# Kernel optimization log

Measured on AMD Instinct MI355X. Metric: run time of the kernel, lower is better.

## Reference

```python
import jax, jax.numpy as jnp
import numpy as np

BETA = 0.25


def setup_inputs() -> dict:
    key = jax.random.key(0)
    k1, k2, k3, k4 = jax.random.split(key, 4)
    B, D, T, H, W = 2, 256, 8, 32, 32
    K = 8192
    z = jax.random.normal(k1, (B, D, T, H, W), dtype=jnp.float32)
    # nn.init.normal_(embedding.weight, mean=0, std=emb_dim ** -0.5)
    emb_w = jax.random.normal(k2, (K, D), dtype=jnp.float32) * (D ** -0.5)
    # torch Linear default init ~ U(-1/sqrt(in), 1/sqrt(in)); scaled normal is fine for a reference
    w1 = jax.random.normal(k3, (D, D), dtype=jnp.float32) * (D ** -0.5)
    w2 = jax.random.normal(k4, (D, D), dtype=jnp.float32) * (D ** -0.5)
    return {"z": z, "emb_w": emb_w, "w1": w1, "w2": w2}


def reference(z, emb_w, w1, w2):
    B, D, T, H, W = z.shape
    K = emb_w.shape[0]
    # permute to channels-last and flatten: [B,T,H,W,D] -> [N,D]
    z_cl = jnp.transpose(z, (0, 2, 3, 4, 1))
    z_flat = z_cl.reshape(-1, D)
    N = z_flat.shape[0]
    # simvq: Linear -> GELU (exact) -> Linear, both bias-free
    quant_codebook = jax.nn.gelu(emb_w @ w1.T, approximate=False) @ w2.T  # [K, D]
    # pairwise squared L2 distances [N, K]
    d = (
        jnp.sum(z_flat ** 2, axis=1, keepdims=True)
        + jnp.sum(quant_codebook ** 2, axis=1)
        - 2.0 * (z_flat @ quant_codebook.T)
    )
    mean_distance = jnp.mean(d)
    idx = jnp.argmin(d, axis=1)  # [N]
    # gather == one-hot @ codebook
    z_q_flat = quant_codebook[idx]  # [N, D]
    z_q = z_q_flat.reshape(z_cl.shape)
    # VQ loss with stop-gradients
    loss = jnp.mean((jax.lax.stop_gradient(z_q) - z_cl) ** 2) + BETA * jnp.mean(
        (z_q - jax.lax.stop_gradient(z_cl)) ** 2
    )
    # straight-through estimator
    z_q = z_cl + jax.lax.stop_gradient(z_q - z_cl)
    # perplexity from code usage histogram (== mean of one-hot encodings)
    counts = jnp.zeros((K,), dtype=jnp.float32).at[idx].add(1.0)
    e_mean = counts / N
    perplexity = jnp.exp(-jnp.sum(e_mean * jnp.log(e_mean + 1e-10)))
    # back to channels-first [B, D, T, H, W]
    z_q = jnp.transpose(z_q, (0, 4, 1, 2, 3))
    return z_q, loss, perplexity, mean_distance
```

## Files before the change

### kernel.cpp

```cpp
#include <hip/hip_runtime.h>
#include <math.h>

#define BATCH 2
#define DIM   256
#define THW   8192
#define NTOK  16384
#define KCB   8192
#define OUTQ  4194304
#define CAP   2000000
#define SCAP  5600

typedef short short8 __attribute__((ext_vector_type(8)));
typedef float f32x4 __attribute__((ext_vector_type(4)));

__device__ __forceinline__ unsigned short f2bf_rn(float v) {
    unsigned u = __float_as_uint(v);
    unsigned r = u + 0x7FFFu + ((u >> 16) & 1u);
    return (unsigned short)(r >> 16);
}
__device__ __forceinline__ float bf2f(unsigned short b) {
    return __uint_as_float((unsigned)b << 16);
}
__device__ __forceinline__ void gl2lds16(const unsigned short* g, unsigned short* l) {
    __builtin_amdgcn_global_load_lds(
        (const __attribute__((address_space(1))) void*)g,
        (__attribute__((address_space(3))) void*)l, 16, 0, 0);
}

__global__ void k_buildA(const float* __restrict__ z,
                         unsigned short* __restrict__ Ahi,
                         unsigned short* __restrict__ Alo,
                         float* __restrict__ zsq,
                         float* __restrict__ sA, float* __restrict__ sB,
                         float* __restrict__ partialZ) {
    __shared__ ushort2 tile[64][65];
    __shared__ float zacc[64];
    __shared__ float lacc[64];
    __shared__ float pz[256];
    int t = threadIdx.x;
    int n0 = blockIdx.x * 64;
    int b = n0 >> 13;
    int thw0 = n0 & 8191;
    if (t < 64) { zacc[t] = 0.f; lacc[t] = 0.f; }
    pz[t] = 0.f;
    __syncthreads();
    int nn_r = t & 63, dg = t >> 6;
    float a1 = 0.f, a2 = 0.f;
    for (int dc = 0; dc < 256; dc += 64) {
        for (int r = 0; r < 16; ++r) {
            int dd = r * 4 + dg;
            float v = z[((size_t)(b * 256 + dc + dd)) * 8192 + thw0 + nn_r];
            unsigned short hb = f2bf_rn(v);
            float hf = bf2f(hb);
            unsigned short lb = f2bf_rn(v - hf);
            float lf = bf2f(lb);
            tile[dd][nn_r] = make_ushort2(hb, lb);
            a1 += v * v;
            a2 += lf * lf;
        }
        __syncthreads();
        int kk = t & 63, ng = t >> 6;
        float dimsum = 0.f;
        for (int i2 = 0; i2 < 16; ++i2) {
            int nn = ng + i2 * 4;
            ushort2 hl = tile[kk][nn];
            size_t base = (size_t)(n0 + nn) * 256;
            Ahi[base + dc + kk] = hl.x;
            Alo[base + dc + kk] = hl.y;
            dimsum += bf2f(hl.x) + bf2f(hl.y);
        }
        atomicAdd(&pz[dc + kk], dimsum);
        __syncthreads();
    }
    atomicAdd(&zacc[nn_r], a1);
    atomicAdd(&lacc[nn_r], a2);
    __syncthreads();
    if (t < 64) {
        zsq[n0 + t] = zacc[t];
        sA[n0 + t] = 2.1f * sqrtf(lacc[t]);
        sB[n0 + t] = 2.1f * sqrtf(zacc[t]);
    }
    partialZ[blockIdx.x * 256 + t] = pz[t];
}

__global__ void k_splitW(const float* __restrict__ w1, const float* __restrict__ w2,
                         unsigned short* __restrict__ W1s, unsigned short* __restrict__ W2s) {
    int bid = blockIdx.x;
    int row = bid & 255;
    const float* src = (bid >> 8) ? w2 : w1;
    unsigned short* dst = ((bid >> 8) ? W2s : W1s) + (size_t)row * 768;
    int t = threadIdx.x;
    float v = src[row * 256 + t];
    unsigned short hb = f2bf_rn(v);
    unsigned short lb = f2bf_rn(v - bf2f(hb));
    dst[t] = hb;
    dst[256 + t] = hb;
    dst[512 + t] = lb;
}

__global__ void k_buildE(const float* __restrict__ emb, unsigned short* __restrict__ E) {
    int t = threadIdx.x;
    int row = blockIdx.x * 4 + (t >> 6);
    int e4 = (t & 63) * 4;
    float4 v = *(const float4*)&emb[(size_t)row * 256 + e4];
    ushort4 hi, lo;
    hi.x = f2bf_rn(v.x); lo.x = f2bf_rn(v.x - bf2f(hi.x));
    hi.y = f2bf_rn(v.y); lo.y = f2bf_rn(v.y - bf2f(hi.y));
    hi.z = f2bf_rn(v.z); lo.z = f2bf_rn(v.z - bf2f(hi.z));
    hi.w = f2bf_rn(v.w); lo.w = f2bf_rn(v.w - bf2f(hi.w));
    size_t base = (size_t)row * 768;
    *(ushort4*)&E[base + e4] = hi;
    *(ushort4*)&E[base + 256 + e4] = lo;
    *(ushort4*)&E[base + 512 + e4] = hi;
}

template <int GELU>
__global__ __launch_bounds__(256) void k_mlp(const unsigned short* __restrict__ A,
                                             const unsigned short* __restrict__ B,
                                             unsigned short* __restrict__ Hs,
                                             float* __restrict__ C_t) {
    __shared__ __align__(16) char smem[32768];
    unsigned short* Asm = (unsigned short*)smem;
    unsigned short* Bsm = (unsigned short*)(smem + 16384);

    int t = threadIdx.x;
    int lane = t & 63;
    int w = t >> 6;
    int wm = w >> 1, wn = w & 1;
    int m0 = blockIdx.y * 128;
    int n0 = blockIdx.x * 128;

    int rA = w * 8 + (lane >> 3);
    int ch_l = lane & 7;
    int ch_g = ch_l ^ (lane >> 3);
    const unsigned short* gA = A + (size_t)(m0 + rA) * 768 + ch_g * 8;
    const unsigned short* gB = B + (size_t)(n0 + rA) * 768 + ch_g * 8;
    unsigned short* lA = &Asm[rA * 64 + ch_l * 8];
    unsigned short* lB = &Bsm[rA * 64 + ch_l * 8];

    f32x4 acc[4][4];
#pragma unroll
    for (int i = 0; i < 4; ++i)
#pragma unroll
        for (int j = 0; j < 4; ++j)
            acc[i][j] = f32x4{0.f, 0.f, 0.f, 0.f};

#pragma unroll
    for (int i = 0; i < 4; ++i) {
        gl2lds16(gA + (size_t)(32 * i) * 768, lA + 32 * i * 64);
        gl2lds16(gB + (size_t)(32 * i) * 768, lB + 32 * i * 64);
    }
    __syncthreads();

    int l15 = lane & 15;
    int quad = lane >> 4;
    int sw = l15 & 7;
    for (int kc = 0; kc < 12; ++kc) {
#pragma unroll
        for (int kk = 0; kk < 2; ++kk) {
            short8 a[4], b[4];
#pragma unroll
            for (int i = 0; i < 4; ++i)
                a[i] = *(const short8*)&Asm[(wm * 64 + i * 16 + l15) * 64 +
                                            (((kk * 4 + quad) ^ sw) * 8)];
#pragma unroll
            for (int j = 0; j < 4; ++j)
                b[j] = *(const short8*)&Bsm[(wn * 64 + j * 16 + l15) * 64 +
                                            (((kk * 4 + quad) ^ sw) * 8)];
#pragma unroll
            for (int i = 0; i < 4; ++i)
#pragma unroll
                for (int j = 0; j < 4; ++j)
                    acc[i][j] = __builtin_amdgcn_mfma_f32_16x16x32_bf16(a[i], b[j], acc[i][j], 0, 0, 0);
        }
        __syncthreads();
        if (kc < 11) {
            int ko = (kc + 1) * 64;
#pragma unroll
            for (int i = 0; i < 4; ++i) {
                gl2lds16(gA + (size_t)(32 * i) * 768 + ko, lA + 32 * i * 64);
                gl2lds16(gB + (size_t)(32 * i) * 768 + ko, lB + 32 * i * 64);
            }
            __syncthreads();
        }
    }

#pragma unroll
    for (int i = 0; i < 4; ++i) {
#pragma unroll
        for (int reg = 0; reg < 4; ++reg) {
            int mrow = m0 + wm * 64 + i * 16 + quad * 4 + reg;
#pragma unroll
            for (int j = 0; j < 4; ++j) {
                int ncol = n0 + wn * 64 + j * 16 + l15;
                float h = acc[i][j][reg];
                if (GELU) {
                    float g = 0.5f * h * (1.f + erff(h * 0.70710678118654752f));
                    unsigned short hb = f2bf_rn(g);
                    unsigned short lb = f2bf_rn(g - bf2f(hb));
                    size_t base = (size_t)mrow * 768;
                    Hs[base + ncol] = hb;
                    Hs[base + 256 + ncol] = lb;
                    Hs[base + 512 + ncol] = hb;
                } else {
                    C_t[(size_t)mrow * 8192 + ncol] = h;
                }
            }
        }
    }
}

__global__ void k_buildB(const float* __restrict__ C_t,
                         unsigned short* __restrict__ Bhi,
                         unsigned short* __restrict__ Blo,
                         float* __restrict__ csq,
                         float* __restrict__ sC, float* __restrict__ sCl,
                         unsigned* __restrict__ tileMaxC, unsigned* __restrict__ tileMaxCl,
                         float* __restrict__ accums, float* __restrict__ partialC) {
    __shared__ ushort2 tile[64][65];
    __shared__ float kacc[64];
    __shared__ float lacc[64];
    __shared__ float pc[256];
    int t = threadIdx.x;
    int k0 = blockIdx.x * 64;
    if (t < 64) { kacc[t] = 0.f; lacc[t] = 0.f; }
    pc[t] = 0.f;
    __syncthreads();
    int nn_r = t & 63, dg = t >> 6;
    float a1 = 0.f, a2 = 0.f;
    for (int dc = 0; dc < 256; dc += 64) {
        for (int r = 0; r < 16; ++r) {
            int dd = r * 4 + dg;
            float v = C_t[(size_t)(dc + dd) * KCB + k0 + nn_r];
            unsigned short hb = f2bf_rn(v);
            float hf = bf2f(hb);
            unsigned short lb = f2bf_rn(v - hf);
            float lf = bf2f(lb);
            tile[dd][nn_r] = make_ushort2(hb, lb);
            a1 += v * v;
            a2 += lf * lf;
        }
        __syncthreads();
        int kk = t & 63, ng = t >> 6;
        float dimsum = 0.f;
        for (int i2 = 0; i2 < 16; ++i2) {
            int nn = ng + i2 * 4;
            ushort2 hl = tile[kk][nn];
            size_t base = (size_t)(k0 + nn) * 256;
            Bhi[base + dc + kk] = hl.x;
            Blo[base + dc + kk] = hl.y;
            dimsum += bf2f(hl.x) + bf2f(hl.y);
        }
        atomicAdd(&pc[dc + kk], dimsum);
        __syncthreads();
    }
    atomicAdd(&kacc[nn_r], a1);
    atomicAdd(&lacc[nn_r], a2);
    __syncthreads();
    if (t < 64) {
        float c2 = kacc[t], l2 = lacc[t];
        float sc = sqrtf(c2), sl = sqrtf(l2);
        csq[k0 + t] = c2;
        sC[k0 + t] = sc;
        sCl[k0 + t] = sl;
        int tl = blockIdx.x >> 1;
        atomicMax(&tileMaxC[tl], __float_as_uint(sc));
        atomicMax(&tileMaxCl[tl], __float_as_uint(sl));
        atomicMax((unsigned*)&accums[3], __float_as_uint(c2));
        atomicMax((unsigned*)&accums[4], __float_as_uint(l2));
    }
    partialC[blockIdx.x * 256 + t] = pc[t];
}

__global__ __launch_bounds__(512, 2) void k_dist_hi(const unsigned short* __restrict__ A,
                                                    const unsigned short* __restrict__ B,
                                                    const float* __restrict__ zsq,
                                                    const float* __restrict__ csq,
                                                    const float* __restrict__ sA,
                                                    const float* __restrict__ sB,
                                                    const unsigned* __restrict__ tileMaxC,
                                                    const unsigned* __restrict__ tileMaxCl,
                                                    unsigned long long* __restrict__ packed,
                                                    float* __restrict__ accums,
                                                    unsigned long long* __restrict__ cand) {
    __shared__ __align__(16) char smem[98304];
    float* sbd     = (float*)smem;
    float* gprev_s = (float*)(smem + 2048);
    float* thr     = (float*)(smem + 3072);
    unsigned* scnt  = (unsigned*)(smem + 4096);
    unsigned* sbase = (unsigned*)(smem + 4100);
    unsigned long long* scand = (unsigned long long*)(smem + 4112);

    int t = threadIdx.x;
    int lane = t & 63;
    int w = t >> 6;
    int wm = w >> 1, wn = w & 1;

    unsigned f = blockIdx.x + (blockIdx.y << 6);
    unsigned xcd = f & 7, i5 = f >> 3;
    unsigned mb = (xcd & 3) * 16 + (i5 & 15);
    unsigned nb = (xcd >> 2) * 16 + (i5 >> 4);
    int m0 = (int)mb * 256;
    int n0 = (int)nb * 256;

    int rsrow = t >> 2;
    int rch = (t & 3) ^ (rsrow & 3);
    const unsigned short* gA0 = A + (size_t)(m0 + rsrow) * 256 + rch * 8;
    const unsigned short* gB0 = B + (size_t)(n0 + rsrow) * 256 + rch * 8;
    unsigned short* smemU = (unsigned short*)smem;

    int l15 = lane & 15;
    int quad = lane >> 4;
    int sw2 = l15 & 3;

    float M1 = sqrtf(accums[3]);
    float M2 = sqrtf(accums[4]);
    float msC  = fmaxf(__uint_as_float(tileMaxC[2 * nb]),
                       __uint_as_float(tileMaxC[2 * nb + 1]));
    float msCl = fmaxf(__uint_as_float(tileMaxCl[2 * nb]),
                       __uint_as_float(tileMaxCl[2 * nb + 1]));

    f32x4 acc[4][8];
#pragma unroll
    for (int i = 0; i < 4; ++i)
#pragma unroll
        for (int j = 0; j < 8; ++j)
            acc[i][j] = f32x4{0.f, 0.f, 0.f, 0.f};

#define STAGE(b, koff)                                                      \
    {                                                                       \
        unsigned short* base_ = smemU + (b) * 16384;                        \
        gl2lds16(gA0 + (koff), base_ + t * 8);                              \
        gl2lds16(gA0 + 128 * 256 + (koff), base_ + 4096 + t * 8);           \
        gl2lds16(gB0 + (koff), base_ + 8192 + t * 8);                       \
        gl2lds16(gB0 + 128 * 256 + (koff), base_ + 12288 + t * 8);          \
    }

#define KSTEP(KC, BUF, WN, DOSTAGE)                                         \
    {                                                                       \
        __builtin_amdgcn_sched_barrier(0);                                  \
        __builtin_amdgcn_s_barrier();   \
        __builtin_amdgcn_sched_barrier(0);                                  \
        if (DOSTAGE) STAGE(((KC) + 2) % 3, ((KC) + 2) * 32);                \
        asm volatile("s_waitcnt vmcnt(" #WN ")" ::: "memory");              \
        __builtin_amdgcn_sched_barrier(0);                                  \
        __builtin_amdgcn_s_barrier();           \
        __builtin_amdgcn_sched_barrier(0);                                  \
        const unsigned short* Ar = smemU + (BUF) * 16384;                   \
        const unsigned short* Br = Ar + 8192;                               \
        short8 a[4], b[8];                                                  \
        _Pragma("unroll")                                                   \
        for (int i = 0; i < 4; ++i)                                         \
            a[i] = *(const short8*)&Ar[(wm * 64 + i * 16 + l15) * 32 +      \
                                       ((quad ^ sw2) * 8)];                 \
        _Pragma("unroll")                                                   \
        for (int j = 0; j < 8; ++j)                                         \
            b[j] = *(const short8*)&Br[(wn * 128 + j * 16 + l15) * 32 +     \
                                       ((quad ^ sw2) * 8)];                 \
        __builtin_amdgcn_s_setprio(1);                                      \
        _Pragma("unroll")                                                   \
        for (int i = 0; i < 4; ++i)                                         \
            _Pragma("unroll")                                               \
            for (int j = 0; j < 8; ++j)                                     \
                acc[i][j] = __builtin_amdgcn_mfma_f32_16x16x32_bf16(        \
                    a[i], b[j], acc[i][j], 0, 0, 0);                        \
        __builtin_amdgcn_s_setprio(0);                                      \
    }

    STAGE(0, 0)
    STAGE(1, 32)
    KSTEP(0, 0, 8, 1)
    KSTEP(1, 1, 8, 1)
    KSTEP(2, 2, 8, 1)
    KSTEP(3, 0, 8, 1)
    KSTEP(4, 1, 8, 1)
    KSTEP(5, 2, 8, 1)
    KSTEP(6, 0, 4, 0)
    KSTEP(7, 1, 0, 0)
#undef KSTEP
#undef STAGE
    __syncthreads();

    float cv[8];
    int cols[8];
#pragma unroll
    for (int j = 0; j < 8; ++j) {
        int cloc = wn * 128 + j * 16 + l15;
        cols[j] = n0 + cloc;
        cv[j] = csq[cols[j]];
    }

    if (t == 0) *scnt = 0;
    if (t < 256) {
        const unsigned* hp = (const unsigned*)&packed[m0 + t];
        gprev_s[t] = __uint_as_float(__atomic_load_n(hp + 1, __ATOMIC_RELAXED));
    }
#pragma unroll
    for (int i = 0; i < 4; ++i) {
#pragma unroll
        for (int reg = 0; reg < 4; ++reg) {
            int rloc = wm * 64 + i * 16 + quad * 4 + reg;
            float zs = zsq[m0 + rloc];
            float bd = 3.4e38f;
#pragma unroll
            for (int j = 0; j < 8; ++j) {
                float d = (zs + cv[j]) - 2.0f * acc[i][j][reg];
                acc[i][j][reg] = d;
                bd = fminf(bd, d);
            }
#pragma unroll
            for (int off = 1; off < 16; off <<= 1)
                bd = fminf(bd, __shfl_xor(bd, off, 64));
            if (l15 == 0) sbd[wn * 256 + rloc] = bd;
        }
    }
    __syncthreads();
    if (t < 256) {
        float bd = fminf(sbd[t], sbd[256 + t]);
        atomicMin(&packed[m0 + t], (unsigned long long)__float_as_uint(bd) << 32);
        float g = fminf(bd, gprev_s[t]);
        thr[t] = g + 1e-3f + sA[m0 + t] * (M1 + msC) + sB[m0 + t] * (M2 + msCl);
    }
    __syncthreads();
    unsigned* cnt = (unsigned*)&accums[2];
#pragma unroll
    for (int i = 0; i < 4; ++i) {
#pragma unroll
        for (int reg = 0; reg < 4; ++reg) {
            int rloc = wm * 64 + i * 16 + quad * 4 + reg;
            float tr = thr[rloc];
            bool p[8];
            bool any = false;
#pragma unroll
            for (int j = 0; j < 8; ++j) {
                p[j] = acc[i][j][reg] <= tr;
                any |= p[j];
            }
            if (__ballot(any)) {
                unsigned rbits = (unsigned)((m0 + rloc) << 13);
#pragma unroll
                for (int j = 0; j < 8; ++j) {
                    if (p[j]) {
                        unsigned long long entry =
                            ((unsigned long long)__float_as_uint(acc[i][j][reg]) << 32) |
                            (rbits | (unsigned)cols[j]);
                        unsigned pos = atomicAdd(scnt, 1u);
                        if (pos < SCAP) scand[pos] = entry;
                        else {
                            unsigned gp2 = atomicAdd(cnt, 1u);
                            if (gp2 < CAP) cand[gp2] = entry;
                        }
                    }
                }
            }
        }
    }
    __syncthreads();
    if (t == 0) {
        unsigned m = *scnt;
        if (m > SCAP) m = SCAP;
        *scnt = m;
        *sbase = atomicAdd(cnt, m);
    }
    __syncthreads();
    {
        unsigned m = *scnt, b0 = *sbase;
        for (unsigned u = t; u < m; u += 512)
            if (b0 + u < CAP) cand[b0 + u] = scand[u];
    }
}

__global__ __launch_bounds__(256) void k_rescore(const unsigned long long* __restrict__ cand,
                                                 const unsigned short* __restrict__ Ahi,
                                                 const unsigned short* __restrict__ Alo,
                                                 const unsigned short* __restrict__ Bhi,
                                                 const unsigned short* __restrict__ Blo,
                                                 const float* __restrict__ zsq,
                                                 const float* __restrict__ csq,
                                                 const float* __restrict__ sA,
                                                 const float* __restrict__ sB,
                                                 const float* __restrict__ sC,
                                                 const float* __restrict__ sCl,
                                                 const unsigned long long* __restrict__ packed,
                                                 unsigned long long* __restrict__ packed2,
                                                 const float* __restrict__ accums) {
    unsigned total = *(const unsigned*)&accums[2];
    if (total > CAP) total = CAP;
    float M1 = sqrtf(accums[3]);
    float M2 = sqrtf(accums[4]);
    int lane = threadIdx.x & 63;
    unsigned wv = blockIdx.x * 4 + (threadIdx.x >> 6);
    unsigned nw = gridDim.x * 4;
    for (unsigned e = wv; e < total; e += nw) {
        unsigned long long ent = cand[e];
        float dhi = __uint_as_float((unsigned)(ent >> 32));
        unsigned nk = (unsigned)ent;
        int n = (nk >> 13) & 16383;
        int k = nk & 8191;
        float g = __uint_as_float((unsigned)(packed[n] >> 32));
        float marg = g + 1e-3f + sA[n] * (M1 + sC[k]) + sB[n] * (M2 + sCl[k]);
        if (dhi > marg) continue;
        ushort4 zh = *((const ushort4*)(Ahi + (size_t)n * 256) + lane);
        ushort4 zl = *((const ushort4*)(Alo + (size_t)n * 256) + lane);
        ushort4 ch = *((const ushort4*)(Bhi + (size_t)k * 256) + lane);
        ushort4 cl = *((const ushort4*)(Blo + (size_t)k * 256) + lane);
        float s = (bf2f(zh.x) + bf2f(zl.x)) * (bf2f(ch.x) + bf2f(cl.x))
                + (bf2f(zh.y) + bf2f(zl.y)) * (bf2f(ch.y) + bf2f(cl.y))
                + (bf2f(zh.z) + bf2f(zl.z)) * (bf2f(ch.z) + bf2f(cl.z))
                + (bf2f(zh.w) + bf2f(zl.w)) * (bf2f(ch.w) + bf2f(cl.w));
#pragma unroll
        for (int off = 1; off < 64; off <<= 1)
            s += __shfl_xor(s, off, 64);
        if (lane == 0) {
            float dd = (zsq[n] + csq[k]) - 2.0f * s;
            unsigned long long p =
                ((unsigned long long)__float_as_uint(dd) << 32) | (unsigned)k;
            atomicMin(&packed2[n], p);
        }
    }
}

__global__ void k_unpack(const unsigned long long* __restrict__ packed2,
                         int* __restrict__ idx, int* __restrict__ counts) {
    int n = blockIdx.x * 256 + threadIdx.x;
    unsigned long long p = packed2[n];
    int k = (int)(p & 0xffffffffull);
    idx[n] = k;
    atomicAdd(&counts[k], 1);
}

__global__ void k_zqloss(const float* __restrict__ z, const float* __restrict__ C_t,
                         const int* __restrict__ idx, float* __restrict__ out,
                         float* __restrict__ loss_sum) {
    __shared__ float red[256];
    int bid = blockIdx.x;
    int b = bid >> 8;
    int d = bid & 255;
    int t = threadIdx.x;
    const float* crow = C_t + (size_t)d * KCB;
    const int* ib = idx + b * THW;
    size_t base = ((size_t)(b * DIM + d)) * THW;
    float lsum = 0.f;
    for (int it = 0; it < 32; ++it) {
        int thw = it * 256 + t;
        int id = ib[thw];
        float v = crow[id];
        float zz = z[base + thw];
        out[base + thw] = v;
        float df = v - zz;
        lsum += df * df;
    }
    red[t] = lsum;
    __syncthreads();
    for (int s = 128; s > 0; s >>= 1) {
        if (t < s) red[t] += red[t + s];
        __syncthreads();
    }
    if (t == 0) atomicAdd(loss_sum, red[0]);
}

__global__ void k_scalars(const int* __restrict__ counts,
                          const float* __restrict__ accums,
                          const float* __restrict__ zsq, const float* __restrict__ csq,
                          const float* __restrict__ partialZ,
                          const float* __restrict__ partialC,
                          float* __restrict__ out_tail) {
    __shared__ double redd[256];
    __shared__ float redf[256];
    int t = threadIdx.x;
    double szsq = 0.0, scsq = 0.0;
    for (int n = t; n < NTOK; n += 256) szsq += (double)zsq[n];
    for (int k = t; k < KCB; k += 256) scsq += (double)csq[k];
    float SZ = 0.f, SC = 0.f;
    for (int b2 = 0; b2 < 256; ++b2) SZ += partialZ[b2 * 256 + t];
    for (int b2 = 0; b2 < 128; ++b2) SC += partialC[b2 * 256 + t];
    double total = 8192.0 * szsq + 16384.0 * scsq - 2.0 * (double)SZ * (double)SC;
    redd[t] = total;
    float s = 0.f;
    for (int k = t; k < KCB; k += 256) {
        float e = (float)counts[k] * (1.0f / 16384.0f);
        s += e * logf(e + 1e-10f);
    }
    redf[t] = s;
    __syncthreads();
    for (int st = 128; st > 0; st >>= 1) {
        if (t < st) { redd[t] += redd[t + st]; redf[t] += redf[t + st]; }
        __syncthreads();
    }
    if (t == 0) {
        out_tail[0] = 1.25f * accums[1] / 4194304.0f;
        out_tail[1] = expf(-redf[0]);
        out_tail[2] = (float)(redd[0] / (16384.0 * 8192.0));
    }
}

extern "C" void kernel_launch(void* const* d_in, const int* in_sizes, int n_in,
                              void* d_out, int out_size, void* d_ws, size_t ws_size,
                              hipStream_t stream) {
    const float* z     = (const float*)d_in[0];
    const float* emb_w = (const float*)d_in[1];
    const float* w1    = (const float*)d_in[2];
    const float* w2    = (const float*)d_in[3];
    float* out = (float*)d_out;

    char* w = (char*)d_ws;
    unsigned short* Ahi = (unsigned short*)(w + 0);
    unsigned short* Alo = (unsigned short*)(w + 8388608);
    unsigned short* Ebf = (unsigned short*)(w + 16777216);
    unsigned short* Bhi = (unsigned short*)(w + 29360128);
    unsigned short* Blo = (unsigned short*)(w + 33554432);
    unsigned short* W1s = (unsigned short*)(w + 37748736);
    unsigned short* W2s = (unsigned short*)(w + 38141952);
    float* zsq   = (float*)(w + 38535168);
    float* sA    = (float*)(w + 38666240);
    float* sB    = (float*)(w + 38731776);
    float* csq   = (float*)(w + 38797312);
    float* sC    = (float*)(w + 38862848);
    float* sCl   = (float*)(w + 38895616);
    unsigned long long* packed  = (unsigned long long*)(w + 38928384);
    unsigned long long* packed2 = (unsigned long long*)(w + 39059456);
    int*   idx    = (int*)(w + 39190528);
    int*   counts = (int*)(w + 39256064);
    float* partialZ = (float*)(w + 39288832);
    float* partialC = (float*)(w + 39550976);
    unsigned* tileMaxC  = (unsigned*)(w + 39682048);
    unsigned* tileMaxCl = (unsigned*)(w + 39682304);
    float* accums = (float*)(w + 39682560);

    float* C_t = (float*)Ebf;
    unsigned short* Hs = (unsigned short*)d_out;
    unsigned long long* cand = (unsigned long long*)d_out;

    hipMemsetAsync(counts, 0, 32768, stream);
    hipMemsetAsync(tileMaxC, 0, 1024, stream);
    hipMemsetAsync(packed, 0xFF, 262144, stream);

    k_buildA<<<NTOK / 64, 256, 0, stream>>>(z, Ahi, Alo, zsq, sA, sB, partialZ);
    k_splitW<<<512, 256, 0, stream>>>(w1, w2, W1s, W2s);
    k_buildE<<<KCB / 4, 256, 0, stream>>>(emb_w, Ebf);

    k_mlp<1><<<dim3(2, KCB / 128), 256, 0, stream>>>(Ebf, W1s, Hs, nullptr);
    k_mlp<0><<<dim3(KCB / 128, 2), 256, 0, stream>>>(W2s, Hs, nullptr, C_t);

    k_buildB<<<KCB / 64, 256, 0, stream>>>(C_t, Bhi, Blo, csq, sC, sCl,
                                           tileMaxC, tileMaxCl, accums, partialC);

    k_dist_hi<<<dim3(NTOK / 256, KCB / 256), 512, 0, stream>>>(
        Ahi, Bhi, zsq, csq, sA, sB, tileMaxC, tileMaxCl, packed, accums, cand);

    k_rescore<<<1024, 256, 0, stream>>>(cand, Ahi, Alo, Bhi, Blo, zsq, csq,
                                        sA, sB, sC, sCl, packed, packed2, accums);

    k_unpack<<<NTOK / 256, 256, 0, stream>>>(packed2, idx, counts);
    k_zqloss<<<BATCH * DIM, 256, 0, stream>>>(z, C_t, idx, out, accums + 1);
    k_scalars<<<1, 256, 0, stream>>>(counts, accums, zsq, csq, partialZ, partialC, out + OUTQ);
}
```

Baseline: 401.7 us.

## Switch distance GEMM to double-buffered 64-wide K chunks with 8-way swizzle

The distance kernel's main loop moves from a triple-buffered pipeline over eight K-chunks of 32 to a double-buffered pipeline over four K-chunks of 64. Each chunk now runs two MFMA sub-steps, and the LDS swizzle widens from 4 to 8 columns. This halves the number of block barriers and stage issues per tile and uses larger global-to-LDS copies. In exchange, shared memory per block rises from 96KB to 128KB, which may limit residency at two blocks per CU, and only two buffers remain to hide load latency.

```diff
diff --git a/kernel.cpp b/kernel.cpp
--- a/kernel.cpp
+++ b/kernel.cpp
@@ -283,7 +283,7 @@
                                                     unsigned long long* __restrict__ packed,
                                                     float* __restrict__ accums,
                                                     unsigned long long* __restrict__ cand) {
-    __shared__ __align__(16) char smem[98304];
+    __shared__ __align__(16) char smem[131072];
     float* sbd     = (float*)smem;
     float* gprev_s = (float*)(smem + 2048);
     float* thr     = (float*)(smem + 3072);
@@ -303,15 +303,18 @@
     int m0 = (int)mb * 256;
     int n0 = (int)nb * 256;
 
-    int rsrow = t >> 2;
-    int rch = (t & 3) ^ (rsrow & 3);
-    const unsigned short* gA0 = A + (size_t)(m0 + rsrow) * 256 + rch * 8;
-    const unsigned short* gB0 = B + (size_t)(n0 + rsrow) * 256 + rch * 8;
+    int rA0 = w * 8 + (lane >> 3);
+    int ch_l = lane & 7;
+    int ch_g = ch_l ^ (lane >> 3);
+    const unsigned short* gA = A + (size_t)(m0 + rA0) * 256 + ch_g * 8;
+    const unsigned short* gB = B + (size_t)(n0 + rA0) * 256 + ch_g * 8;
     unsigned short* smemU = (unsigned short*)smem;
+    unsigned short* lA = smemU + rA0 * 64 + ch_l * 8;
+    unsigned short* lB = smemU + 16384 + rA0 * 64 + ch_l * 8;
 
     int l15 = lane & 15;
     int quad = lane >> 4;
-    int sw2 = l15 & 3;
+    int sw = l15 & 7;
 
     float M1 = sqrtf(accums[3]);
     float M2 = sqrtf(accums[4]);
@@ -327,13 +330,17 @@
         for (int j = 0; j < 8; ++j)
             acc[i][j] = f32x4{0.f, 0.f, 0.f, 0.f};
 
-#define STAGE(b, koff)                                                      \
+#define STAGE(B_, KO)                                                       \
     {                                                                       \
-        unsigned short* base_ = smemU + (b) * 16384;                        \
-        gl2lds16(gA0 + (koff), base_ + t * 8);                              \
-        gl2lds16(gA0 + 128 * 256 + (koff), base_ + 4096 + t * 8);           \
-        gl2lds16(gB0 + (koff), base_ + 8192 + t * 8);                       \
-        gl2lds16(gB0 + 128 * 256 + (koff), base_ + 12288 + t * 8);          \
+        int off_ = (B_) * 32768;                                            \
+        _Pragma("unroll")                                                   \
+        for (int i_ = 0; i_ < 4; ++i_)                                      \
+            gl2lds16(gA + (size_t)(64 * i_) * 256 + (KO),                   \
+                     lA + off_ + 64 * i_ * 64);                             \
+        _Pragma("unroll")                                                   \
+        for (int i_ = 0; i_ < 4; ++i_)                                      \
+            gl2lds16(gB + (size_t)(64 * i_) * 256 + (KO),                   \
+                     lB + off_ + 64 * i_ * 64);                             \
     }
 
 #define KSTEP(KC, BUF, WN, DOSTAGE)                                         \
@@ -341,42 +348,40 @@
         __builtin_amdgcn_sched_barrier(0);                                  \
         __builtin_amdgcn_s_barrier();   \
         __builtin_amdgcn_sched_barrier(0);                                  \
-        if (DOSTAGE) STAGE(((KC) + 2) % 3, ((KC) + 2) * 32);                \
+        if (DOSTAGE) STAGE((BUF) ^ 1, ((KC) + 1) * 64);                     \
         asm volatile("s_waitcnt vmcnt(" #WN ")" ::: "memory");              \
         __builtin_amdgcn_sched_barrier(0);                                  \
-        __builtin_amdgcn_s_barrier();           \
+        __builtin_amdgcn_s_barrier();            \
         __builtin_amdgcn_sched_barrier(0);                                  \
-        const unsigned short* Ar = smemU + (BUF) * 16384;                   \
-        const unsigned short* Br = Ar + 8192;                               \
-        short8 a[4], b[8];                                                  \
+        const unsigned short* Ar = smemU + (BUF) * 32768;                   \
+        const unsigned short* Br = Ar + 16384;                              \
         _Pragma("unroll")                                                   \
-        for (int i = 0; i < 4; ++i)                                         \
-            a[i] = *(const short8*)&Ar[(wm * 64 + i * 16 + l15) * 32 +      \
-                                       ((quad ^ sw2) * 8)];                 \
-        _Pragma("unroll")                                                   \
-        for (int j = 0; j < 8; ++j)                                         \
-            b[j] = *(const short8*)&Br[(wn * 128 + j * 16 + l15) * 32 +     \
-                                       ((quad ^ sw2) * 8)];                 \
-        __builtin_amdgcn_s_setprio(1);                                      \
-        _Pragma("unroll")                                                   \
-        for (int i = 0; i < 4; ++i)                                         \
+        for (int kk = 0; kk < 2; ++kk) {                                    \
+            short8 a[4], b[8];                                              \
+            _Pragma("unroll")                                               \
+            for (int i = 0; i < 4; ++i)                                     \
+                a[i] = *(const short8*)&Ar[(wm * 64 + i * 16 + l15) * 64 +  \
+                                           (((kk * 4 + quad) ^ sw) * 8)];   \
             _Pragma("unroll")                                               \
             for (int j = 0; j < 8; ++j)                                     \
-                acc[i][j] = __builtin_amdgcn_mfma_f32_16x16x32_bf16(        \
-                    a[i], b[j], acc[i][j], 0, 0, 0);                        \
-        __builtin_amdgcn_s_setprio(0);                                      \
+                b[j] = *(const short8*)&Br[(wn * 128 + j * 16 + l15) * 64 + \
+                                           (((kk * 4 + quad) ^ sw) * 8)];   \
+            __builtin_amdgcn_s_setprio(1);                                  \
+            _Pragma("unroll")                                               \
+            for (int i = 0; i < 4; ++i)                                     \
+                _Pragma("unroll")                                           \
+                for (int j = 0; j < 8; ++j)                                 \
+                    acc[i][j] = __builtin_amdgcn_mfma_f32_16x16x32_bf16(    \
+                        a[i], b[j], acc[i][j], 0, 0, 0);                    \
+            __builtin_amdgcn_s_setprio(0);                                  \
+        }                                                                   \
     }
 
     STAGE(0, 0)
-    STAGE(1, 32)
     KSTEP(0, 0, 8, 1)
     KSTEP(1, 1, 8, 1)
-    KSTEP(2, 2, 8, 1)
-    KSTEP(3, 0, 8, 1)
-    KSTEP(4, 1, 8, 1)
-    KSTEP(5, 2, 8, 1)
-    KSTEP(6, 0, 4, 0)
-    KSTEP(7, 1, 0, 0)
+    KSTEP(2, 0, 8, 1)
+    KSTEP(3, 1, 0, 0)
 #undef KSTEP
 #undef STAGE
     __syncthreads();
```

Result: no change. 401.6 us (-0.0%).
